# Kernel optimization log

Hardware: AMD Instinct MI355X
Metric: run time of the kernel (lower is better)

The kernel has to match this reference:

```python
import jax, jax.numpy as jnp
import numpy as np

B=1; NW=8; SEG=511; S=NW*(SEG+1); W=256; C=S//W; H=12; D=64; DM=768; FF=3072; V=50265; L=12; OUT=128; G=NW
SCALE = float(1.0/np.sqrt(D))
GPOS = np.arange(NW)*(S//NW)                      # global (CLS) token positions
IDX = np.arange(C)[:,None]*W + np.arange(3*W)[None,:]   # [C,3W] gather into padded key seq
_band = np.abs(np.arange(3*W)[None,:]-np.arange(W)[:,None]-W) <= W   # [W,3W] |rel|<=W band
_kpos = IDX - W
LMASK = _band[None] & ((_kpos>=0)&(_kpos<S))[:,None,:]  # [C,W,3W]

def _ln(x, s, b):
    m = jnp.mean(x, -1, keepdims=True)
    v = jnp.mean((x-m)**2, -1, keepdims=True)
    return (x-m)*jax.lax.rsqrt(v+1e-5)*s + b

def _layer(h, Wq,bq,Wk,bk,Wv,bv,Wo,bo,Wqg,bqg,Wkg,bkg,Wvg,bvg,l1s,l1b,W1,b1,W2,b2,l2s,l2b):
    hd = lambda z: z.reshape(B,S,H,D).transpose(0,2,1,3)   # [B,H,S,D]
    q = hd(h@Wq+bq)*SCALE
    k = hd(h@Wk+bk); v = hd(h@Wv+bv)
    kc = jnp.pad(k, ((0,0),(0,0),(W,W),(0,0)))[:,:,IDX]    # [B,H,C,3W,D]
    vc = jnp.pad(v, ((0,0),(0,0),(W,W),(0,0)))[:,:,IDX]
    qc = q.reshape(B,H,C,W,D)
    # banded local scores + scores to global keys, joint softmax (HF longformer style)
    sl = jnp.where(LMASK, jnp.einsum('bhcqd,bhckd->bhcqk', qc, kc), -1e9)
    sg = jnp.einsum('bhcqd,bhgd->bhcqg', qc, k[:,:,GPOS])
    a = jax.nn.softmax(jnp.concatenate([sg, sl], -1), -1)  # [B,H,C,W,G+3W]
    out = jnp.einsum('bhcqg,bhgd->bhcqd', a[..., :G], v[:,:,GPOS]) \
        + jnp.einsum('bhcqk,bhckd->bhcqd', a[..., G:], vc)
    out = out.reshape(B,H,S,D)
    # global tokens: full attention with separate global projections, overwrite their outputs
    qg = (h[:,GPOS]@Wqg+bqg).reshape(B,G,H,D).transpose(0,2,1,3)*SCALE
    ag = jax.nn.softmax(jnp.einsum('bhgd,bhsd->bhgs', qg, hd(h@Wkg+bkg)), -1)
    out = out.at[:,:,GPOS,:].set(jnp.einsum('bhgs,bhsd->bhgd', ag, hd(h@Wvg+bvg)))
    y = out.transpose(0,2,1,3).reshape(B,S,DM)@Wo + bo
    h = _ln(h + y, l1s, l1b)
    return _ln(h + jax.nn.gelu(h@W1+b1)@W2 + b2, l2s, l2b)

def setup_inputs() -> dict:
    keys = iter(jax.random.split(jax.random.key(0), 64))
    p = lambda *s: jax.random.normal(next(keys), s, jnp.float32)*0.02
    d = {"x": jax.random.randint(next(keys), (B, NW*SEG), 0, V),
         "word_emb": p(V, DM), "pos_emb": p(S, DM),
         "emb_ln_s": jnp.ones((DM,)), "emb_ln_b": jnp.zeros((DM,))}
    for n in ["Wq","Wk","Wv","Wo","Wqg","Wkg","Wvg"]:
        d[n] = p(L, DM, DM); d["b"+n[1:]] = jnp.zeros((L, DM))
    d["ln1_s"]=jnp.ones((L,DM)); d["ln1_b"]=jnp.zeros((L,DM))
    d["W1"]=p(L,DM,FF); d["b1"]=jnp.zeros((L,FF))
    d["W2"]=p(L,FF,DM); d["b2"]=jnp.zeros((L,DM))
    d["ln2_s"]=jnp.ones((L,DM)); d["ln2_b"]=jnp.zeros((L,DM))
    d["Wout"]=p(DM,OUT); d["bout"]=jnp.zeros((OUT,))
    return d

def reference(x, word_emb, pos_emb, emb_ln_s, emb_ln_b, Wq, bq, Wk, bk, Wv, bv, Wo, bo,
              Wqg, bqg, Wkg, bkg, Wvg, bvg, ln1_s, ln1_b, W1, b1, W2, b2, ln2_s, ln2_b,
              Wout, bout):
    # prepend CLS (id 0) per window -> S=4096 token ids
    ids = jnp.concatenate([jnp.zeros((B, NW, 1), x.dtype), x.reshape(B, NW, SEG)], 2).reshape(B, S)
    h = _ln(word_emb[ids] + pos_emb[None], emb_ln_s, emb_ln_b)
    for l in range(L):
        h = _layer(h, Wq[l],bq[l],Wk[l],bk[l],Wv[l],bv[l],Wo[l],bo[l],
                   Wqg[l],bqg[l],Wkg[l],bkg[l],Wvg[l],bvg[l],
                   ln1_s[l],ln1_b[l],W1[l],b1[l],W2[l],b2[l],ln2_s[l],ln2_b[l])
    return h[:, GPOS] @ Wout + bout   # cls_pooling + output head: [B, NW, OUT]
```

## Files before the change

### kernel.cpp

```cpp
#include <hip/hip_runtime.h>
#include <hip/hip_bf16.h>


typedef unsigned short u16;
typedef __attribute__((ext_vector_type(4))) float floatx4;
typedef __attribute__((ext_vector_type(4))) unsigned int uintx4;
typedef __attribute__((ext_vector_type(8))) short bf16x8;
typedef __attribute__((ext_vector_type(4))) u16 u16x4;

#define S_LEN 4096
#define QKVG_N 4608
#define NL 12

__device__ inline u16 f2bf(float x) {
    union { __hip_bfloat16 b; u16 u; } cv;
    cv.b = __float2bfloat16(x);
    return cv.u;
}
__device__ inline float bf2f(u16 u) {
    union { float f; unsigned int i; } c; c.i = ((unsigned int)u) << 16; return c.f;
}
__device__ inline float gelu_f(float x) {
    float x3 = x * x * x;
    return 0.5f * x * (1.0f + tanhf(0.7978845608028654f * (x + 0.044715f * x3)));
}

#define GLDS16(g, l)                                                              \
    __builtin_amdgcn_global_load_lds(                                             \
        (const __attribute__((address_space(1))) unsigned int*)(g),               \
        (__attribute__((address_space(3))) unsigned int*)(l), 16, 0, 0)

__global__ __launch_bounds__(256) void prep_weights_k(
    const float* __restrict__ Wq0, const float* __restrict__ Wk0, const float* __restrict__ Wv0,
    const float* __restrict__ Wkg0, const float* __restrict__ Wvg0, const float* __restrict__ Wqg0,
    const float* __restrict__ Wo0, const float* __restrict__ W10, const float* __restrict__ W20,
    const float* __restrict__ bq0, const float* __restrict__ bk0, const float* __restrict__ bv0,
    const float* __restrict__ bkg0, const float* __restrict__ bvg0, const float* __restrict__ bqg0,
    u16* __restrict__ wTall, float* __restrict__ bcatall)
{
    const int l = blockIdx.y;
    const size_t sqo = (size_t)l * 589824;
    const size_t sff = (size_t)l * 2359296;
    u16* wqkvgT = wTall + (size_t)l * 8847360;
    u16* woT = wqkvgT + 3538944;
    u16* w1T = woT + 589824;
    u16* w2T = w1T + 2359296;

    int bid = blockIdx.x;
    int t = threadIdx.x;
    if (bid >= 2160) {
        int i = (bid - 2160) * 256 + t;
        float v;
        if (i < 768)       v = bq0[l * 768 + i];
        else if (i < 1536) v = bk0[l * 768 + i - 768];
        else if (i < 2304) v = bv0[l * 768 + i - 1536];
        else if (i < 3072) v = bkg0[l * 768 + i - 2304];
        else if (i < 3840) v = bvg0[l * 768 + i - 3072];
        else               v = bqg0[l * 768 + i - 3840];
        bcatall[(size_t)l * 4608 + i] = v;
        return;
    }
    const float* src; u16* dst; int K, N, tile;
    if (bid < 864) {
        int m = bid / 144; tile = bid % 144;
        src = ((m == 0) ? Wq0 : (m == 1) ? Wk0 : (m == 2) ? Wv0 :
               (m == 3) ? Wkg0 : (m == 4) ? Wvg0 : Wqg0) + sqo;
        dst = wqkvgT + (size_t)m * 589824;
        K = 768; N = 768;
    } else if (bid < 1008) { tile = bid - 864;  src = Wo0 + sqo; dst = woT; K = 768;  N = 768; }
    else if (bid < 1584)   { tile = bid - 1008; src = W10 + sff; dst = w1T; K = 768;  N = 3072; }
    else                   { tile = bid - 1584; src = W20 + sff; dst = w2T; K = 3072; N = 768; }

    int nt = N >> 6;
    int k0 = (tile / nt) << 6, n0 = (tile % nt) << 6;
    __shared__ float tb[64][65];
    int r = t >> 4, c4 = (t & 15) * 4;
    #pragma unroll
    for (int j = 0; j < 4; j++) {
        int kk = r + j * 16;
        floatx4 v = *(const floatx4*)&src[(size_t)(k0 + kk) * N + n0 + c4];
        #pragma unroll
        for (int i = 0; i < 4; i++) tb[c4 + i][kk] = v[i];
    }
    __syncthreads();
    int k4 = (t & 15) * 4, nb = t >> 4;
    #pragma unroll
    for (int j = 0; j < 4; j++) {
        int n = nb + j * 16;
        u16x4 o;
        #pragma unroll
        for (int i = 0; i < 4; i++) o[i] = f2bf(tb[n][k4 + i]);
        *(u16x4*)&dst[(size_t)(n0 + n) * K + k0 + k4] = o;
    }
}

template <int ACT, int WF, int WB, int SKIPQG, int WVT, int SPLITB>
__global__ __launch_bounds__(256, 3) void gemm_k(
    const u16* __restrict__ A, const u16* __restrict__ Bt,
    const float* __restrict__ bias,
    float* __restrict__ Cf, u16* __restrict__ Cb, u16* __restrict__ vTg,
    int N, int K, int lda, int ldb)
{
    int lin = blockIdx.y * 32 + blockIdx.x;
    int qq = gridDim.y << 2;
    int wg = (lin & 7) * qq + (lin >> 3);
    int bx = wg & 31, by = wg >> 5;
    if (SKIPQG && by >= 30 && (bx & 3) != 0) return;
    int bm = bx * 128, bn = by * 128;
    const int zoff = SPLITB ? blockIdx.z : 0;
    const u16* Ab = A + (size_t)zoff * K;
    const u16* Bb = Bt + (size_t)zoff * K;
    float* Cfz = WF ? Cf + (size_t)zoff * S_LEN * N : (float*)nullptr;

    __shared__ __align__(16) u16 As[128][64];
    __shared__ __align__(16) u16 Bs[128][64];
    int t = threadIdx.x, lane = t & 63, wv = t >> 6;
    int wm = (wv >> 1) * 64, wn = (wv & 1) * 64;
    int srow = t >> 3, scol = (t & 7) * 8;
    int fr = lane & 15, fo = (lane >> 4) * 8;

    floatx4 acc[4][4];
    #pragma unroll
    for (int i = 0; i < 4; i++)
        #pragma unroll
        for (int j = 0; j < 4; j++) acc[i][j] = (floatx4){0.f, 0.f, 0.f, 0.f};

    const int nk = K >> 6;
    for (int kt = 0; kt < nk; ++kt) {
        const u16* ag = Ab + (size_t)(bm + srow) * lda + kt * 64 + scol;
        const u16* bg = Bb + (size_t)(bn + srow) * ldb + kt * 64 + scol;
        #pragma unroll
        for (int c = 0; c < 4; ++c) {
            GLDS16(ag + (size_t)(32 * c) * lda, &As[srow + 32 * c][scol]);
            GLDS16(bg + (size_t)(32 * c) * ldb, &Bs[srow + 32 * c][scol]);
        }
        __syncthreads();
        #pragma unroll
        for (int ks = 0; ks < 2; ++ks) {
            bf16x8 af[4], bfr[4];
            #pragma unroll
            for (int i = 0; i < 4; i++) af[i]  = *(const bf16x8*)&As[wm + i * 16 + fr][ks * 32 + fo];
            #pragma unroll
            for (int i = 0; i < 4; i++) bfr[i] = *(const bf16x8*)&Bs[wn + i * 16 + fr][ks * 32 + fo];
            #pragma unroll
            for (int i = 0; i < 4; i++)
                #pragma unroll
                for (int j = 0; j < 4; j++)
                    acc[i][j] = __builtin_amdgcn_mfma_f32_16x16x32_bf16(af[i], bfr[j], acc[i][j], 0, 0, 0);
        }
        __syncthreads();
    }

    int dr = (lane >> 4) * 4, dc = lane & 15;
    #pragma unroll
    for (int i = 0; i < 4; i++) {
        #pragma unroll
        for (int j = 0; j < 4; j++) {
            int r0 = bm + wm + i * 16 + dr;
            int cc = bn + wn + j * 16 + dc;
            float bsv = (!SPLITB || blockIdx.z == 0) ? bias[cc] : 0.f;
            u16x4 tv;
            #pragma unroll
            for (int r = 0; r < 4; r++) {
                float v = acc[i][j][r] + bsv;
                if (ACT == 1) v = gelu_f(v);
                if (WF) Cfz[(size_t)(r0 + r) * N + cc] = v;
                if (WB) { u16 b = f2bf(v); Cb[(size_t)(r0 + r) * N + cc] = b; tv[r] = b; }
            }
            if (WVT && cc >= 1536 && cc < 2304)
                *(u16x4*)&vTg[(size_t)(cc - 1536) * 4096 + r0] = tv;
        }
    }
}

__global__ __launch_bounds__(256) void attn_local_k(
    const u16* __restrict__ qkvg, const u16* __restrict__ vTg, u16* __restrict__ aob)
{
    int lin = blockIdx.y * 64 + blockIdx.x;
    int wg = (lin & 7) * 96 + (lin >> 3);
    const int qb = wg & 63, hh = wg >> 6;
    const int t = threadIdx.x, lane = t & 63, w = t >> 6;
    const int g = lane >> 4, qi = lane & 15;
    __shared__ __align__(16) u16 ks[64][72];
    __shared__ __align__(16) u16 vt[64][72];
    __shared__ __align__(16) u16 pbuf[4][16][40];

    const int q0w = qb * 64 + w * 16;
    const int sq = q0w + qi;

    bf16x8 qf0, qf1;
    {
        const u16* qp = qkvg + (size_t)(q0w + qi) * QKVG_N + hh * 64 + g * 8;
        qf0 = *(const bf16x8*)qp;
        qf1 = *(const bf16x8*)(qp + 32);
    }

    floatx4 acc[4];
    #pragma unroll
    for (int i = 0; i < 4; i++) acc[i] = (floatx4){0.f, 0.f, 0.f, 0.f};
    float mrun = -1e30f, lrun = 0.f;

    for (int tile = 0; tile <= 9; ++tile) {
        const int kbase = qb * 64 - 256 + (tile - 1) * 64;
        if (tile > 0 && (kbase < 0 || kbase >= S_LEN)) continue;
        __syncthreads();
        if (tile == 0) {
            for (int i = t; i < 576; i += 256) ((uintx4*)vt)[i] = (uintx4){0, 0, 0, 0};
            __syncthreads();
            if (t < 64) {
                int gg = t >> 3, d0 = (t & 7) * 8;
                *(uintx4*)&ks[gg][d0] =
                    *(const uintx4*)(qkvg + (size_t)(gg * 512) * QKVG_N + 768 + hh * 64 + d0);
            }
            for (int e = t; e < 512; e += 256) {
                int d = e >> 3, gg = e & 7;
                vt[d][gg] = vTg[(size_t)(hh * 64 + d) * 4096 + gg * 512];
            }
        } else {
            for (int c = t; c < 512; c += 256) {
                int r = c >> 3, c0 = (c & 7) * 8;
                *(uintx4*)&ks[r][c0] =
                    *(const uintx4*)(qkvg + (size_t)(kbase + r) * QKVG_N + 768 + hh * 64 + c0);
                *(uintx4*)&vt[r][c0] =
                    *(const uintx4*)(vTg + (size_t)(hh * 64 + r) * 4096 + kbase + c0);
            }
        }
        __syncthreads();

        const bool gt = (tile == 0);
        const bool edge = (tile == 1) | (tile == 9);
        const int ng = gt ? 1 : 2;
        for (int kg2 = 0; kg2 < ng; ++kg2) {
            floatx4 sf[2];
            sf[1] = (floatx4){0.f, 0.f, 0.f, 0.f};
            {
                bf16x8 ka0 = *(const bf16x8*)&ks[kg2 * 32 + qi][g * 8];
                bf16x8 ka1 = *(const bf16x8*)&ks[kg2 * 32 + qi][32 + g * 8];
                floatx4 z = (floatx4){0.f, 0.f, 0.f, 0.f};
                z = __builtin_amdgcn_mfma_f32_16x16x32_bf16(ka0, qf0, z, 0, 0, 0);
                sf[0] = __builtin_amdgcn_mfma_f32_16x16x32_bf16(ka1, qf1, z, 0, 0, 0);
            }
            if (!gt) {
                bf16x8 kb0 = *(const bf16x8*)&ks[kg2 * 32 + 16 + qi][g * 8];
                bf16x8 kb1 = *(const bf16x8*)&ks[kg2 * 32 + 16 + qi][32 + g * 8];
                floatx4 z = (floatx4){0.f, 0.f, 0.f, 0.f};
                z = __builtin_amdgcn_mfma_f32_16x16x32_bf16(kb0, qf0, z, 0, 0, 0);
                sf[1] = __builtin_amdgcn_mfma_f32_16x16x32_bf16(kb1, qf1, z, 0, 0, 0);
            }
            float p8[8];
            float mloc = -1e30f;
            #pragma unroll
            for (int f = 0; f < 2; ++f)
                #pragma unroll
                for (int r = 0; r < 4; ++r) {
                    int kl = kg2 * 32 + f * 16 + g * 4 + r;
                    float sc = sf[f][r] * 0.125f;
                    if (gt) {
                        if (kl >= 8) sc = -1e30f;
                    } else if (edge) {
                        int dd = kbase + kl - sq;
                        if (dd > 256 || dd < -256) sc = -1e30f;
                    }
                    p8[f * 4 + r] = sc;
                    mloc = fmaxf(mloc, sc);
                }
            mloc = fmaxf(mloc, __shfl_xor(mloc, 16));
            mloc = fmaxf(mloc, __shfl_xor(mloc, 32));
            float mnew = fmaxf(mrun, mloc);
            float alpha = __expf(mrun - mnew);
            mrun = mnew;
            float ls = 0.f;
            #pragma unroll
            for (int i = 0; i < 8; ++i) { float p = __expf(p8[i] - mnew); p8[i] = p; ls += p; }
            ls += __shfl_xor(ls, 16);
            ls += __shfl_xor(ls, 32);
            lrun = lrun * alpha + ls;
            u16x4 w0, w1;
            #pragma unroll
            for (int r = 0; r < 4; ++r) { w0[r] = f2bf(p8[r]); w1[r] = f2bf(p8[4 + r]); }
            *(u16x4*)&pbuf[w][qi][g * 4] = w0;
            *(u16x4*)&pbuf[w][qi][16 + g * 4] = w1;
            float al[4];
            #pragma unroll
            for (int r = 0; r < 4; ++r) al[r] = __shfl(alpha, g * 4 + r);
            #pragma unroll
            for (int dt = 0; dt < 4; ++dt)
                #pragma unroll
                for (int r = 0; r < 4; ++r) acc[dt][r] *= al[r];
            bf16x8 pf = *(const bf16x8*)&pbuf[w][qi][g * 8];
            #pragma unroll
            for (int dt = 0; dt < 4; ++dt) {
                bf16x8 vb = *(const bf16x8*)&vt[dt * 16 + qi][kg2 * 32 + g * 8];
                acc[dt] = __builtin_amdgcn_mfma_f32_16x16x32_bf16(pf, vb, acc[dt], 0, 0, 0);
            }
        }
    }

    float inv = 1.f / lrun;
    float li[4];
    #pragma unroll
    for (int r = 0; r < 4; ++r) li[r] = __shfl(inv, g * 4 + r);
    #pragma unroll
    for (int dt = 0; dt < 4; ++dt)
        #pragma unroll
        for (int r = 0; r < 4; ++r) {
            int s = q0w + g * 4 + r;
            aob[(size_t)s * 768 + hh * 64 + dt * 16 + qi] = f2bf(acc[dt][r] * li[r]);
        }
}

#define BLOCK_MEANVAR(sum, sq, mean, inv)                                        \
    {                                                                            \
        for (int o_ = 32; o_ > 0; o_ >>= 1) {                                    \
            sum += __shfl_down(sum, o_); sq += __shfl_down(sq, o_);              \
        }                                                                        \
        __shared__ float rs_[4], rq_[4];                                         \
        if ((threadIdx.x & 63) == 0) { rs_[threadIdx.x >> 6] = sum; rq_[threadIdx.x >> 6] = sq; } \
        __syncthreads();                                                         \
        float S_ = rs_[0] + rs_[1] + rs_[2] + rs_[3];                            \
        float Q_ = rq_[0] + rq_[1] + rq_[2] + rq_[3];                            \
        mean = S_ * (1.f / 768.f);                                               \
        float var_ = Q_ * (1.f / 768.f) - mean * mean;                           \
        inv = rsqrtf(var_ + 1e-5f);                                              \
    }

__global__ __launch_bounds__(256) void embed_ln_k(
    const int* __restrict__ x, const float* __restrict__ wemb, const float* __restrict__ pemb,
    const float* __restrict__ gs, const float* __restrict__ gb,
    float* __restrict__ hf, u16* __restrict__ hb)
{
    int s = blockIdx.x, t = threadIdx.x;
    int w = s >> 9, p = s & 511;
    int id = (p == 0) ? 0 : x[w * 511 + p - 1];
    float v[3], sum = 0.f, sq = 0.f;
    #pragma unroll
    for (int r = 0; r < 3; r++) {
        int d = t + r * 256;
        float e = wemb[(size_t)id * 768 + d] + pemb[(size_t)s * 768 + d];
        v[r] = e; sum += e; sq += e * e;
    }
    float mean, inv;
    BLOCK_MEANVAR(sum, sq, mean, inv)
    #pragma unroll
    for (int r = 0; r < 3; r++) {
        int d = t + r * 256;
        float y = (v[r] - mean) * inv * gs[d] + gb[d];
        hf[(size_t)s * 768 + d] = y;
        hb[(size_t)s * 768 + d] = f2bf(y);
    }
}

__global__ __launch_bounds__(256) void ln_resid_k(
    const float* __restrict__ xa, const float* __restrict__ xb, const float* __restrict__ xc,
    const float* __restrict__ gs, const float* __restrict__ gb,
    float* __restrict__ of, u16* __restrict__ ob)
{
    int s = blockIdx.x, t = threadIdx.x;
    const float* pa = xa + (size_t)s * 768;
    const float* pb = xb + (size_t)s * 768;
    const float* pc = xc + (size_t)s * 768;
    float v[3], sum = 0.f, sq = 0.f;
    #pragma unroll
    for (int r = 0; r < 3; r++) {
        int d = t + r * 256;
        float e = pa[d] + pb[d] + pc[d];
        v[r] = e; sum += e; sq += e * e;
    }
    float mean, inv;
    BLOCK_MEANVAR(sum, sq, mean, inv)
    #pragma unroll
    for (int r = 0; r < 3; r++) {
        int d = t + r * 256;
        float y = (v[r] - mean) * inv * gs[d] + gb[d];
        of[(size_t)s * 768 + d] = y;
        ob[(size_t)s * 768 + d] = f2bf(y);
    }
}

__global__ __launch_bounds__(256) void attn_gpart_k(
    const u16* __restrict__ qkvg,
    float* __restrict__ pacc, float* __restrict__ pm, float* __restrict__ pl)
{
    const int hh = blockIdx.x, ck = blockIdx.y;
    const int t = threadIdx.x;
    __shared__ float qs[8][64];
    __shared__ __align__(16) u16 ks[128][72];
    __shared__ __align__(16) u16 vs[128][64];
    __shared__ float sc[8][128];
    __shared__ float mred[8], lred[8];

    for (int i = t; i < 512; i += 256) {
        int g = i >> 6, d = i & 63;
        qs[g][d] = bf2f(qkvg[(size_t)(g * 512) * QKVG_N + 3840 + hh * 64 + d]) * 0.125f;
    }
    const int s0 = ck * 128;
    for (int u = t; u < 1024; u += 256) {
        int r = u >> 3, c = u & 7;
        const u16* src = qkvg + (size_t)(s0 + r) * QKVG_N + hh * 64 + c * 8;
        *(uintx4*)&ks[r][c * 8] = *(const uintx4*)(src + 2304);
        *(uintx4*)&vs[r][c * 8] = *(const uintx4*)(src + 3072);
    }
    __syncthreads();

    {
        int key = t & 127, q0 = (t >> 7) * 4;
        float a[4] = {0.f, 0.f, 0.f, 0.f};
        #pragma unroll
        for (int c = 0; c < 8; ++c) {
            uintx4 pk = *(const uintx4*)&ks[key][c * 8];
            const u16* uu = (const u16*)&pk;
            #pragma unroll
            for (int e = 0; e < 8; ++e) {
                float kv = bf2f(uu[e]);
                #pragma unroll
                for (int q = 0; q < 4; ++q) a[q] += kv * qs[q0 + q][c * 8 + e];
            }
        }
        #pragma unroll
        for (int q = 0; q < 4; ++q) sc[q0 + q][key] = a[q];
    }
    __syncthreads();

    {
        int q = t >> 5, lq = t & 31;
        float m = -1e30f;
        #pragma unroll
        for (int i = 0; i < 4; ++i) m = fmaxf(m, sc[q][lq + i * 32]);
        #pragma unroll
        for (int o = 1; o < 32; o <<= 1) m = fmaxf(m, __shfl_xor(m, o));
        float ls = 0.f;
        #pragma unroll
        for (int i = 0; i < 4; ++i) {
            float p = __expf(sc[q][lq + i * 32] - m);
            sc[q][lq + i * 32] = p; ls += p;
        }
        #pragma unroll
        for (int o = 1; o < 32; o <<= 1) ls += __shfl_xor(ls, o);
        if (lq == 0) { mred[q] = m; lred[q] = ls; }
    }
    __syncthreads();

    {
        int d = t & 63, qb = t >> 6;
        float a0 = 0.f, a1 = 0.f;
        #pragma unroll 4
        for (int s = 0; s < 128; ++s) {
            float v = bf2f(vs[s][d]);
            a0 += sc[qb][s] * v;
            a1 += sc[qb + 4][s] * v;
        }
        float* pb = pacc + (((size_t)hh * 32 + ck) * 8) * 64;
        pb[qb * 64 + d] = a0;
        pb[(qb + 4) * 64 + d] = a1;
        if (t < 8) {
            pm[((size_t)hh * 32 + ck) * 8 + t] = mred[t];
            pl[((size_t)hh * 32 + ck) * 8 + t] = lred[t];
        }
    }
}

__global__ __launch_bounds__(64) void attn_gred_k(
    const float* __restrict__ pacc, const float* __restrict__ pm,
    const float* __restrict__ pl, u16* __restrict__ aob)
{
    int hh = blockIdx.x, gq = blockIdx.y;
    int d = threadIdx.x;
    float M = -1e30f;
    #pragma unroll 4
    for (int c = 0; c < 32; ++c)
        M = fmaxf(M, pm[((size_t)hh * 32 + c) * 8 + gq]);
    float L = 0.f, o = 0.f;
    #pragma unroll 4
    for (int c = 0; c < 32; ++c) {
        float w = __expf(pm[((size_t)hh * 32 + c) * 8 + gq] - M);
        L += pl[((size_t)hh * 32 + c) * 8 + gq] * w;
        o += w * pacc[(((size_t)hh * 32 + c) * 8 + gq) * 64 + d];
    }
    aob[(size_t)(gq * 512) * 768 + hh * 64 + d] = f2bf(o / L);
}

__global__ __launch_bounds__(128) void head_k(
    const float* __restrict__ hf, const float* __restrict__ Wout,
    const float* __restrict__ bout, float* __restrict__ out)
{
    int g = blockIdx.x, n = threadIdx.x;
    __shared__ float hsh[768];
    for (int i = n; i < 768; i += 128) hsh[i] = hf[(size_t)(g * 512) * 768 + i];
    __syncthreads();
    float a = 0.f;
    #pragma unroll 4
    for (int k = 0; k < 768; k++) a += hsh[k] * Wout[k * 128 + n];
    out[g * 128 + n] = a + bout[n];
}

extern "C" void kernel_launch(void* const* d_in, const int* in_sizes, int n_in,
                              void* d_out, int out_size, void* d_ws, size_t ws_size,
                              hipStream_t stream)
{
    (void)in_sizes; (void)n_in; (void)out_size; (void)ws_size;
    const int*   x    = (const int*)  d_in[0];
    const float* wemb = (const float*)d_in[1];
    const float* pemb = (const float*)d_in[2];
    const float* elns = (const float*)d_in[3];
    const float* elnb = (const float*)d_in[4];
    const float* Wq   = (const float*)d_in[5];
    const float* bq   = (const float*)d_in[6];
    const float* Wk   = (const float*)d_in[7];
    const float* bk   = (const float*)d_in[8];
    const float* Wv   = (const float*)d_in[9];
    const float* bv   = (const float*)d_in[10];
    const float* Wo   = (const float*)d_in[11];
    const float* bo   = (const float*)d_in[12];
    const float* Wqg  = (const float*)d_in[13];
    const float* bqg  = (const float*)d_in[14];
    const float* Wkg  = (const float*)d_in[15];
    const float* bkg  = (const float*)d_in[16];
    const float* Wvg  = (const float*)d_in[17];
    const float* bvg  = (const float*)d_in[18];
    const float* l1s  = (const float*)d_in[19];
    const float* l1b  = (const float*)d_in[20];
    const float* W1   = (const float*)d_in[21];
    const float* b1   = (const float*)d_in[22];
    const float* W2   = (const float*)d_in[23];
    const float* b2   = (const float*)d_in[24];
    const float* l2s  = (const float*)d_in[25];
    const float* l2b  = (const float*)d_in[26];
    const float* Wout = (const float*)d_in[27];
    const float* boutp= (const float*)d_in[28];

    char* W = (char*)d_ws;
    float* hf    = (float*)(W);
    u16*   hb    = (u16*)  (W + 12582912);
    u16*   qkvg  = (u16*)  (W + 18874368);
    u16*   vTg   = (u16*)  (W + 56623104);
    u16*   aob   = (u16*)  (W + 62914560);
    float* yf    = (float*)(W + 69206016);
    u16*   ff1b  = (u16*)  (W + 94371840);
    float* pacc  = (float*)(W + 119537664);
    float* pmw   = (float*)(W + 120324096);
    float* plw   = (float*)(W + 120336384);
    float* bcatall = (float*)(W + 120348672);
    u16*   wTall = (u16*)  (W + 120569856);

    prep_weights_k<<<dim3(2178, 12), 256, 0, stream>>>(
        Wq, Wk, Wv, Wkg, Wvg, Wqg, Wo, W1, W2,
        bq, bk, bv, bkg, bvg, bqg, wTall, bcatall);

    embed_ln_k<<<4096, 256, 0, stream>>>(x, wemb, pemb, elns, elnb, hf, hb);

    float* yf0 = yf;
    float* yf1 = yf + (size_t)4096 * 768;

    for (int l = 0; l < NL; ++l) {
        u16* wTl      = wTall + (size_t)l * 8847360;
        u16* wqkvgT_l = wTl;
        u16* woT_l    = wTl + 3538944;
        u16* w1T_l    = woT_l + 589824;
        u16* w2T_l    = w1T_l + 2359296;
        float* bcat_l = bcatall + (size_t)l * 4608;
        const float* bo_l  = bo  + (size_t)l * 768;
        const float* b1_l  = b1  + (size_t)l * 3072;
        const float* b2_l  = b2  + (size_t)l * 768;
        const float* l1s_l = l1s + (size_t)l * 768;
        const float* l1b_l = l1b + (size_t)l * 768;
        const float* l2s_l = l2s + (size_t)l * 768;
        const float* l2b_l = l2b + (size_t)l * 768;

        gemm_k<0, 0, 1, 1, 1, 0><<<dim3(32, 36), 256, 0, stream>>>(
            hb, wqkvgT_l, bcat_l, (float*)nullptr, qkvg, vTg, QKVG_N, 768, 768, 768);

        attn_local_k<<<dim3(64, 12), 256, 0, stream>>>(qkvg, vTg, aob);

        attn_gpart_k<<<dim3(12, 32), 256, 0, stream>>>(qkvg, pacc, pmw, plw);
        attn_gred_k<<<dim3(12, 8), 64, 0, stream>>>(pacc, pmw, plw, aob);

        gemm_k<0, 1, 0, 0, 0, 1><<<dim3(32, 6, 2), 256, 0, stream>>>(
            aob, woT_l, bo_l, yf, (u16*)nullptr, (u16*)nullptr, 768, 384, 768, 768);
        ln_resid_k<<<4096, 256, 0, stream>>>(hf, yf0, yf1, l1s_l, l1b_l, hf, hb);

        gemm_k<1, 0, 1, 0, 0, 0><<<dim3(32, 24), 256, 0, stream>>>(
            hb, w1T_l, b1_l, (float*)nullptr, ff1b, (u16*)nullptr, 3072, 768, 768, 768);
        gemm_k<0, 1, 0, 0, 0, 1><<<dim3(32, 6, 2), 256, 0, stream>>>(
            ff1b, w2T_l, b2_l, yf, (u16*)nullptr, (u16*)nullptr, 768, 1536, 3072, 3072);
        ln_resid_k<<<4096, 256, 0, stream>>>(hf, yf0, yf1, l2s_l, l2b_l, hf, hb);
    }

    head_k<<<8, 128, 0, stream>>>(hf, Wout, boutp, (float*)d_out);
}
```

Measured before the change: 2.900 ms.

## Pipeline weight prep and local-attention loads, fold residual into split-K GEMM epilogue

Three independent changes. The weight-prep kernel becomes a persistent grid-stride loop that prefetches the next tile into registers while the current tile is converted and stored. The local attention kernel computes the valid tile range up front and register-prefetches the next K/V tile so global loads overlap the softmax and MFMA work. The residual add moves into the Wo and W2 split-K GEMM epilogues (applied on the z=0 slice only), so the layer-norm kernel reads two buffers instead of three. These cut memory-latency stalls and one full-tensor read per layer norm, at the cost of more registers in the attention and GEMM kernels.

New measurement: 3.145 ms. +8.5%, slower.

```diff
diff --git a/kernel.cpp b/kernel.cpp
--- a/kernel.cpp
+++ b/kernel.cpp
@@ -38,67 +38,90 @@
     const float* __restrict__ bkg0, const float* __restrict__ bvg0, const float* __restrict__ bqg0,
     u16* __restrict__ wTall, float* __restrict__ bcatall)
 {
-    const int l = blockIdx.y;
-    const size_t sqo = (size_t)l * 589824;
-    const size_t sff = (size_t)l * 2359296;
-    u16* wqkvgT = wTall + (size_t)l * 8847360;
-    u16* woT = wqkvgT + 3538944;
-    u16* w1T = woT + 589824;
-    u16* w2T = w1T + 2359296;
-
-    int bid = blockIdx.x;
-    int t = threadIdx.x;
-    if (bid >= 2160) {
-        int i = (bid - 2160) * 256 + t;
+    const int t = threadIdx.x;
+    const int bid = blockIdx.x;
+    if (bid >= 2048) {
+        int i = (bid - 2048) * 256 + t;
+        int l = i / 4608, j = i - l * 4608;
         float v;
-        if (i < 768)       v = bq0[l * 768 + i];
-        else if (i < 1536) v = bk0[l * 768 + i - 768];
-        else if (i < 2304) v = bv0[l * 768 + i - 1536];
-        else if (i < 3072) v = bkg0[l * 768 + i - 2304];
-        else if (i < 3840) v = bvg0[l * 768 + i - 3072];
-        else               v = bqg0[l * 768 + i - 3840];
-        bcatall[(size_t)l * 4608 + i] = v;
+        if (j < 768)       v = bq0[l * 768 + j];
+        else if (j < 1536) v = bk0[l * 768 + j - 768];
+        else if (j < 2304) v = bv0[l * 768 + j - 1536];
+        else if (j < 3072) v = bkg0[l * 768 + j - 2304];
+        else if (j < 3840) v = bvg0[l * 768 + j - 3072];
+        else               v = bqg0[l * 768 + j - 3840];
+        bcatall[(size_t)l * 4608 + j] = v;
         return;
     }
-    const float* src; u16* dst; int K, N, tile;
-    if (bid < 864) {
-        int m = bid / 144; tile = bid % 144;
-        src = ((m == 0) ? Wq0 : (m == 1) ? Wk0 : (m == 2) ? Wv0 :
-               (m == 3) ? Wkg0 : (m == 4) ? Wvg0 : Wqg0) + sqo;
-        dst = wqkvgT + (size_t)m * 589824;
-        K = 768; N = 768;
-    } else if (bid < 1008) { tile = bid - 864;  src = Wo0 + sqo; dst = woT; K = 768;  N = 768; }
-    else if (bid < 1584)   { tile = bid - 1008; src = W10 + sff; dst = w1T; K = 768;  N = 3072; }
-    else                   { tile = bid - 1584; src = W20 + sff; dst = w2T; K = 3072; N = 768; }
-
-    int nt = N >> 6;
-    int k0 = (tile / nt) << 6, n0 = (tile % nt) << 6;
+
     __shared__ float tb[64][65];
-    int r = t >> 4, c4 = (t & 15) * 4;
-    #pragma unroll
-    for (int j = 0; j < 4; j++) {
-        int kk = r + j * 16;
-        floatx4 v = *(const floatx4*)&src[(size_t)(k0 + kk) * N + n0 + c4];
-        #pragma unroll
-        for (int i = 0; i < 4; i++) tb[c4 + i][kk] = v[i];
-    }
-    __syncthreads();
-    int k4 = (t & 15) * 4, nb = t >> 4;
-    #pragma unroll
-    for (int j = 0; j < 4; j++) {
-        int n = nb + j * 16;
-        u16x4 o;
-        #pragma unroll
-        for (int i = 0; i < 4; i++) o[i] = f2bf(tb[n][k4 + i]);
-        *(u16x4*)&dst[(size_t)(n0 + n) * K + k0 + k4] = o;
-    }
-}
-
-template <int ACT, int WF, int WB, int SKIPQG, int WVT, int SPLITB>
+    const int NT = 25920;
+    const int rr = t >> 4, cc4 = (t & 15) * 4;
+
+    auto decode = [&](int tid, const float*& src, u16*& dst, int& K, int& N,
+                      int& k0, int& n0) {
+        int l = tid / 2160, b = tid - l * 2160;
+        const size_t sqo = (size_t)l * 589824;
+        const size_t sff = (size_t)l * 2359296;
+        u16* wq = wTall + (size_t)l * 8847360;
+        int tile;
+        if (b < 864) {
+            int m = b / 144; tile = b - m * 144;
+            src = ((m == 0) ? Wq0 : (m == 1) ? Wk0 : (m == 2) ? Wv0 :
+                   (m == 3) ? Wkg0 : (m == 4) ? Wvg0 : Wqg0) + sqo;
+            dst = wq + (size_t)m * 589824; K = 768; N = 768;
+        } else if (b < 1008) { tile = b - 864;  src = Wo0 + sqo; dst = wq + 3538944; K = 768;  N = 768; }
+        else if (b < 1584)   { tile = b - 1008; src = W10 + sff; dst = wq + 4128768; K = 768;  N = 3072; }
+        else                 { tile = b - 1584; src = W20 + sff; dst = wq + 6488064; K = 3072; N = 768; }
+        int nt = N >> 6;
+        k0 = (tile / nt) << 6; n0 = (tile % nt) << 6;
+    };
+
+    int tid = bid;
+    const float* src; u16* dst; int K, N, k0, n0;
+    decode(tid, src, dst, K, N, k0, n0);
+    floatx4 rg[4];
+    #pragma unroll
+    for (int j = 0; j < 4; j++)
+        rg[j] = *(const floatx4*)&src[(size_t)(k0 + rr + 16 * j) * N + n0 + cc4];
+
+    for (;;) {
+        #pragma unroll
+        for (int j = 0; j < 4; j++) {
+            int kk = rr + 16 * j;
+            #pragma unroll
+            for (int i = 0; i < 4; i++) tb[cc4 + i][kk] = rg[j][i];
+        }
+        u16* dcur = dst; int Kc = K, k0c = k0, n0c = n0;
+        __syncthreads();
+        int tidn = tid + 2048;
+        bool more = (tidn < NT);
+        if (more) {
+            decode(tidn, src, dst, K, N, k0, n0);
+            #pragma unroll
+            for (int j = 0; j < 4; j++)
+                rg[j] = *(const floatx4*)&src[(size_t)(k0 + rr + 16 * j) * N + n0 + cc4];
+        }
+        #pragma unroll
+        for (int j = 0; j < 4; j++) {
+            int nn = rr + 16 * j;
+            u16x4 o;
+            #pragma unroll
+            for (int i = 0; i < 4; i++) o[i] = f2bf(tb[nn][cc4 + i]);
+            *(u16x4*)&dcur[(size_t)(n0c + nn) * Kc + k0c + cc4] = o;
+        }
+        if (!more) break;
+        tid = tidn;
+        __syncthreads();
+    }
+}
+
+template <int ACT, int WF, int WB, int SKIPQG, int WVT, int SPLITB, int RESID>
 __global__ __launch_bounds__(256, 3) void gemm_k(
     const u16* __restrict__ A, const u16* __restrict__ Bt,
     const float* __restrict__ bias,
     float* __restrict__ Cf, u16* __restrict__ Cb, u16* __restrict__ vTg,
+    const float* __restrict__ Rf,
     int N, int K, int lda, int ldb)
 {
     int lin = blockIdx.y * 32 + blockIdx.x;
@@ -164,6 +187,10 @@
             for (int r = 0; r < 4; r++) {
                 float v = acc[i][j][r] + bsv;
                 if (ACT == 1) v = gelu_f(v);
+                if (RESID) {
+                    if (!SPLITB || blockIdx.z == 0)
+                        v += Rf[(size_t)(r0 + r) * N + cc];
+                }
                 if (WF) Cfz[(size_t)(r0 + r) * N + cc] = v;
                 if (WB) { u16 b = f2bf(v); Cb[(size_t)(r0 + r) * N + cc] = b; tv[r] = b; }
             }
@@ -200,99 +227,121 @@
     for (int i = 0; i < 4; i++) acc[i] = (floatx4){0.f, 0.f, 0.f, 0.f};
     float mrun = -1e30f, lrun = 0.f;
 
-    for (int tile = 0; tile <= 9; ++tile) {
-        const int kbase = qb * 64 - 256 + (tile - 1) * 64;
-        if (tile > 0 && (kbase < 0 || kbase >= S_LEN)) continue;
+    int tlo = 5 - qb; if (tlo < 1) tlo = 1;
+    int thi = 68 - qb; if (thi > 9) thi = 9;
+
+    const int rs = t >> 3, cs = (t & 7) * 8;
+    uintx4 kr0, kr1, vr0, vr1;
+    auto prefetch_local = [&](int kb) {
+        const u16* kp = qkvg + (size_t)(kb + rs) * QKVG_N + 768 + hh * 64 + cs;
+        kr0 = *(const uintx4*)kp;
+        kr1 = *(const uintx4*)(kp + (size_t)32 * QKVG_N);
+        const u16* vp = vTg + (size_t)(hh * 64 + rs) * 4096 + kb + cs;
+        vr0 = *(const uintx4*)vp;
+        vr1 = *(const uintx4*)(vp + (size_t)32 * 4096);
+    };
+
+    auto smax_pv = [&](floatx4 sf0, floatx4 sf1, int kg2, int kbase, int mask,
+                       bool half) {
+        floatx4 sf[2] = {sf0, sf1};
+        float p8[8];
+        float mloc = -1e30f;
+        #pragma unroll
+        for (int f = 0; f < 2; ++f)
+            #pragma unroll
+            for (int r = 0; r < 4; ++r) {
+                int kl = kg2 * 32 + f * 16 + g * 4 + r;
+                float sc = sf[f][r] * 0.125f;
+                if (mask == 1) { if (kl >= 8) sc = -1e30f; }
+                else if (mask == 2) {
+                    int dd = kbase + kl - sq;
+                    if (dd > 256 || dd < -256) sc = -1e30f;
+                }
+                p8[f * 4 + r] = sc;
+                mloc = fmaxf(mloc, sc);
+            }
+        mloc = fmaxf(mloc, __shfl_xor(mloc, 16));
+        mloc = fmaxf(mloc, __shfl_xor(mloc, 32));
+        float mnew = fmaxf(mrun, mloc);
+        float alpha = __expf(mrun - mnew);
+        mrun = mnew;
+        float ls = 0.f;
+        #pragma unroll
+        for (int i = 0; i < 8; ++i) { float p = __expf(p8[i] - mnew); p8[i] = p; ls += p; }
+        ls += __shfl_xor(ls, 16);
+        ls += __shfl_xor(ls, 32);
+        lrun = lrun * alpha + ls;
+        u16x4 w0, w1;
+        #pragma unroll
+        for (int r = 0; r < 4; ++r) { w0[r] = f2bf(p8[r]); w1[r] = f2bf(p8[4 + r]); }
+        *(u16x4*)&pbuf[w][qi][g * 4] = w0;
+        *(u16x4*)&pbuf[w][qi][16 + g * 4] = w1;
+        float al[4];
+        #pragma unroll
+        for (int r = 0; r < 4; ++r) al[r] = __shfl(alpha, g * 4 + r);
+        #pragma unroll
+        for (int dt = 0; dt < 4; ++dt)
+            #pragma unroll
+            for (int r = 0; r < 4; ++r) acc[dt][r] *= al[r];
+        bf16x8 pf = *(const bf16x8*)&pbuf[w][qi][g * 8];
+        #pragma unroll
+        for (int dt = 0; dt < 4; ++dt) {
+            bf16x8 vb = *(const bf16x8*)&vt[dt * 16 + qi][kg2 * 32 + g * 8];
+            acc[dt] = __builtin_amdgcn_mfma_f32_16x16x32_bf16(pf, vb, acc[dt], 0, 0, 0);
+        }
+        (void)half;
+    };
+
+    for (int i = t; i < 576; i += 256) ((uintx4*)vt)[i] = (uintx4){0, 0, 0, 0};
+    __syncthreads();
+    if (t < 64) {
+        int gg = t >> 3, d0 = (t & 7) * 8;
+        *(uintx4*)&ks[gg][d0] =
+            *(const uintx4*)(qkvg + (size_t)(gg * 512) * QKVG_N + 768 + hh * 64 + d0);
+    }
+    for (int e = t; e < 512; e += 256) {
+        int d = e >> 3, gg = e & 7;
+        vt[d][gg] = vTg[(size_t)(hh * 64 + d) * 4096 + gg * 512];
+    }
+    __syncthreads();
+    prefetch_local((qb + tlo - 5) * 64);
+    {
+        bf16x8 ka0 = *(const bf16x8*)&ks[qi][g * 8];
+        bf16x8 ka1 = *(const bf16x8*)&ks[qi][32 + g * 8];
+        floatx4 z = (floatx4){0.f, 0.f, 0.f, 0.f};
+        z = __builtin_amdgcn_mfma_f32_16x16x32_bf16(ka0, qf0, z, 0, 0, 0);
+        floatx4 s0 = __builtin_amdgcn_mfma_f32_16x16x32_bf16(ka1, qf1, z, 0, 0, 0);
+        smax_pv(s0, (floatx4){0.f, 0.f, 0.f, 0.f}, 0, 0, 1, true);
+    }
+
+    for (int tile = tlo; tile <= thi; ++tile) {
+        const int kbase = (qb + tile - 5) * 64;
         __syncthreads();
-        if (tile == 0) {
-            for (int i = t; i < 576; i += 256) ((uintx4*)vt)[i] = (uintx4){0, 0, 0, 0};
-            __syncthreads();
-            if (t < 64) {
-                int gg = t >> 3, d0 = (t & 7) * 8;
-                *(uintx4*)&ks[gg][d0] =
-                    *(const uintx4*)(qkvg + (size_t)(gg * 512) * QKVG_N + 768 + hh * 64 + d0);
-            }
-            for (int e = t; e < 512; e += 256) {
-                int d = e >> 3, gg = e & 7;
-                vt[d][gg] = vTg[(size_t)(hh * 64 + d) * 4096 + gg * 512];
-            }
-        } else {
-            for (int c = t; c < 512; c += 256) {
-                int r = c >> 3, c0 = (c & 7) * 8;
-                *(uintx4*)&ks[r][c0] =
-                    *(const uintx4*)(qkvg + (size_t)(kbase + r) * QKVG_N + 768 + hh * 64 + c0);
-                *(uintx4*)&vt[r][c0] =
-                    *(const uintx4*)(vTg + (size_t)(hh * 64 + r) * 4096 + kbase + c0);
-            }
-        }
+        *(uintx4*)&ks[rs][cs] = kr0;
+        *(uintx4*)&ks[rs + 32][cs] = kr1;
+        *(uintx4*)&vt[rs][cs] = vr0;
+        *(uintx4*)&vt[rs + 32][cs] = vr1;
         __syncthreads();
-
-        const bool gt = (tile == 0);
-        const bool edge = (tile == 1) | (tile == 9);
-        const int ng = gt ? 1 : 2;
-        for (int kg2 = 0; kg2 < ng; ++kg2) {
-            floatx4 sf[2];
-            sf[1] = (floatx4){0.f, 0.f, 0.f, 0.f};
+        if (tile < thi) prefetch_local(kbase + 64);
+        const int mask = ((tile == 1) | (tile == 9)) ? 2 : 0;
+        #pragma unroll
+        for (int kg2 = 0; kg2 < 2; ++kg2) {
+            floatx4 s0, s1;
             {
                 bf16x8 ka0 = *(const bf16x8*)&ks[kg2 * 32 + qi][g * 8];
                 bf16x8 ka1 = *(const bf16x8*)&ks[kg2 * 32 + qi][32 + g * 8];
                 floatx4 z = (floatx4){0.f, 0.f, 0.f, 0.f};
                 z = __builtin_amdgcn_mfma_f32_16x16x32_bf16(ka0, qf0, z, 0, 0, 0);
-                sf[0] = __builtin_amdgcn_mfma_f32_16x16x32_bf16(ka1, qf1, z, 0, 0, 0);
+                s0 = __builtin_amdgcn_mfma_f32_16x16x32_bf16(ka1, qf1, z, 0, 0, 0);
             }
-            if (!gt) {
+            {
                 bf16x8 kb0 = *(const bf16x8*)&ks[kg2 * 32 + 16 + qi][g * 8];
                 bf16x8 kb1 = *(const bf16x8*)&ks[kg2 * 32 + 16 + qi][32 + g * 8];
                 floatx4 z = (floatx4){0.f, 0.f, 0.f, 0.f};
                 z = __builtin_amdgcn_mfma_f32_16x16x32_bf16(kb0, qf0, z, 0, 0, 0);
-                sf[1] = __builtin_amdgcn_mfma_f32_16x16x32_bf16(kb1, qf1, z, 0, 0, 0);
+                s1 = __builtin_amdgcn_mfma_f32_16x16x32_bf16(kb1, qf1, z, 0, 0, 0);
             }
-            float p8[8];
-            float mloc = -1e30f;
-            #pragma unroll
-            for (int f = 0; f < 2; ++f)
-                #pragma unroll
-                for (int r = 0; r < 4; ++r) {
-                    int kl = kg2 * 32 + f * 16 + g * 4 + r;
-                    float sc = sf[f][r] * 0.125f;
-                    if (gt) {
-                        if (kl >= 8) sc = -1e30f;
-                    } else if (edge) {
-                        int dd = kbase + kl - sq;
-                        if (dd > 256 || dd < -256) sc = -1e30f;
-                    }
-                    p8[f * 4 + r] = sc;
-                    mloc = fmaxf(mloc, sc);
-                }
-            mloc = fmaxf(mloc, __shfl_xor(mloc, 16));
-            mloc = fmaxf(mloc, __shfl_xor(mloc, 32));
-            float mnew = fmaxf(mrun, mloc);
-            float alpha = __expf(mrun - mnew);
-            mrun = mnew;
-            float ls = 0.f;
-            #pragma unroll
-            for (int i = 0; i < 8; ++i) { float p = __expf(p8[i] - mnew); p8[i] = p; ls += p; }
-            ls += __shfl_xor(ls, 16);
-            ls += __shfl_xor(ls, 32);
-            lrun = lrun * alpha + ls;
-            u16x4 w0, w1;
-            #pragma unroll
-            for (int r = 0; r < 4; ++r) { w0[r] = f2bf(p8[r]); w1[r] = f2bf(p8[4 + r]); }
-            *(u16x4*)&pbuf[w][qi][g * 4] = w0;
-            *(u16x4*)&pbuf[w][qi][16 + g * 4] = w1;
-            float al[4];
-            #pragma unroll
-            for (int r = 0; r < 4; ++r) al[r] = __shfl(alpha, g * 4 + r);
-            #pragma unroll
-            for (int dt = 0; dt < 4; ++dt)
-                #pragma unroll
-                for (int r = 0; r < 4; ++r) acc[dt][r] *= al[r];
-            bf16x8 pf = *(const bf16x8*)&pbuf[w][qi][g * 8];
-            #pragma unroll
-            for (int dt = 0; dt < 4; ++dt) {
-                bf16x8 vb = *(const bf16x8*)&vt[dt * 16 + qi][kg2 * 32 + g * 8];
-                acc[dt] = __builtin_amdgcn_mfma_f32_16x16x32_bf16(pf, vb, acc[dt], 0, 0, 0);
-            }
+            smax_pv(s0, s1, kg2, kbase, mask, false);
         }
     }
 
@@ -351,19 +400,18 @@
 }
 
 __global__ __launch_bounds__(256) void ln_resid_k(
-    const float* __restrict__ xa, const float* __restrict__ xb, const float* __restrict__ xc,
+    const float* __restrict__ xb, const float* __restrict__ xc,
     const float* __restrict__ gs, const float* __restrict__ gb,
     float* __restrict__ of, u16* __restrict__ ob)
 {
     int s = blockIdx.x, t = threadIdx.x;
-    const float* pa = xa + (size_t)s * 768;
     const float* pb = xb + (size_t)s * 768;
     const float* pc = xc + (size_t)s * 768;
     float v[3], sum = 0.f, sq = 0.f;
     #pragma unroll
     for (int r = 0; r < 3; r++) {
         int d = t + r * 256;
-        float e = pa[d] + pb[d] + pc[d];
+        float e = pb[d] + pc[d];
         v[r] = e; sum += e; sq += e * e;
     }
     float mean, inv;
@@ -542,7 +590,7 @@
     float* bcatall = (float*)(W + 120348672);
     u16*   wTall = (u16*)  (W + 120569856);
 
-    prep_weights_k<<<dim3(2178, 12), 256, 0, stream>>>(
+    prep_weights_k<<<2264, 256, 0, stream>>>(
         Wq, Wk, Wv, Wkg, Wvg, Wqg, Wo, W1, W2,
         bq, bk, bv, bkg, bvg, bqg, wTall, bcatall);
 
@@ -566,23 +614,25 @@
         const float* l2s_l = l2s + (size_t)l * 768;
         const float* l2b_l = l2b + (size_t)l * 768;
 
-        gemm_k<0, 0, 1, 1, 1, 0><<<dim3(32, 36), 256, 0, stream>>>(
-            hb, wqkvgT_l, bcat_l, (float*)nullptr, qkvg, vTg, QKVG_N, 768, 768, 768);
+        gemm_k<0, 0, 1, 1, 1, 0, 0><<<dim3(32, 36), 256, 0, stream>>>(
+            hb, wqkvgT_l, bcat_l, (float*)nullptr, qkvg, vTg, (const float*)nullptr,
+            QKVG_N, 768, 768, 768);
 
         attn_local_k<<<dim3(64, 12), 256, 0, stream>>>(qkvg, vTg, aob);
 
         attn_gpart_k<<<dim3(12, 32), 256, 0, stream>>>(qkvg, pacc, pmw, plw);
         attn_gred_k<<<dim3(12, 8), 64, 0, stream>>>(pacc, pmw, plw, aob);
 
-        gemm_k<0, 1, 0, 0, 0, 1><<<dim3(32, 6, 2), 256, 0, stream>>>(
-            aob, woT_l, bo_l, yf, (u16*)nullptr, (u16*)nullptr, 768, 384, 768, 768);
-        ln_resid_k<<<4096, 256, 0, stream>>>(hf, yf0, yf1, l1s_l, l1b_l, hf, hb);
-
-        gemm_k<1, 0, 1, 0, 0, 0><<<dim3(32, 24), 256, 0, stream>>>(
-            hb, w1T_l, b1_l, (float*)nullptr, ff1b, (u16*)nullptr, 3072, 768, 768, 768);
-        gemm_k<0, 1, 0, 0, 0, 1><<<dim3(32, 6, 2), 256, 0, stream>>>(
-            ff1b, w2T_l, b2_l, yf, (u16*)nullptr, (u16*)nullptr, 768, 1536, 3072, 3072);
-        ln_resid_k<<<4096, 256, 0, stream>>>(hf, yf0, yf1, l2s_l, l2b_l, hf, hb);
+        gemm_k<0, 1, 0, 0, 0, 1, 1><<<dim3(32, 6, 2), 256, 0, stream>>>(
+            aob, woT_l, bo_l, yf, (u16*)nullptr, (u16*)nullptr, hf, 768, 384, 768, 768);
+        ln_resid_k<<<4096, 256, 0, stream>>>(yf0, yf1, l1s_l, l1b_l, hf, hb);
+
+        gemm_k<1, 0, 1, 0, 0, 0, 0><<<dim3(32, 24), 256, 0, stream>>>(
+            hb, w1T_l, b1_l, (float*)nullptr, ff1b, (u16*)nullptr, (const float*)nullptr,
+            3072, 768, 768, 768);
+        gemm_k<0, 1, 0, 0, 0, 1, 1><<<dim3(32, 6, 2), 256, 0, stream>>>(
+            ff1b, w2T_l, b2_l, yf, (u16*)nullptr, (u16*)nullptr, hf, 768, 1536, 3072, 3072);
+        ln_resid_k<<<4096, 256, 0, stream>>>(yf0, yf1, l2s_l, l2b_l, hf, hb);
     }
 
     head_k<<<8, 128, 0, stream>>>(hf, Wout, boutp, (float*)d_out);
```
